# Kernel optimization log

Hardware: AMD Instinct MI355X
Metric: run time of the kernel (lower is better)

Reference implementation:

```python
import jax, jax.numpy as jnp
import numpy as np

EMBED = 1024
HEADS = 16
HEAD_DIM = EMBED // HEADS
HIDDEN = 4 * EMBED
EPS = 1e-6


def setup_inputs() -> dict:
    key = jax.random.key(0)
    ks = jax.random.split(key, 8)
    s = 0.02
    return {
        "x": jax.random.normal(ks[0], (2, 2048, EMBED), dtype=jnp.float32),
        "ln1_w": jnp.ones((EMBED,), jnp.float32),
        "ln1_b": jnp.zeros((EMBED,), jnp.float32),
        "qkv_w": jax.random.normal(ks[1], (3 * EMBED, EMBED), jnp.float32) * s,
        "qkv_b": jnp.zeros((3 * EMBED,), jnp.float32),
        "proj_w": jax.random.normal(ks[2], (EMBED, EMBED), jnp.float32) * s,
        "proj_b": jnp.zeros((EMBED,), jnp.float32),
        "ln2_w": jnp.ones((EMBED,), jnp.float32),
        "ln2_b": jnp.zeros((EMBED,), jnp.float32),
        "fc1_w": jax.random.normal(ks[3], (HIDDEN, EMBED), jnp.float32) * s,
        "fc1_b": jnp.zeros((HIDDEN,), jnp.float32),
        "fc2_w": jax.random.normal(ks[4], (EMBED, HIDDEN), jnp.float32) * s,
        "fc2_b": jnp.zeros((EMBED,), jnp.float32),
    }


def _layernorm(x, w, b):
    mu = jnp.mean(x, axis=-1, keepdims=True)
    var = jnp.mean(jnp.square(x - mu), axis=-1, keepdims=True)
    return (x - mu) * jax.lax.rsqrt(var + EPS) * w + b


def _attn(x, qkv_w, qkv_b, proj_w, proj_b):
    B, S, E = x.shape
    qkv = x @ qkv_w.T + qkv_b                      # [B,S,3E]
    qkv = qkv.reshape(B, S, 3, HEADS, HEAD_DIM)
    q, k, v = jnp.moveaxis(qkv, 2, 0)              # each [B,S,H,D]
    q = q.transpose(0, 2, 1, 3)                    # [B,H,S,D]
    k = k.transpose(0, 2, 1, 3)
    v = v.transpose(0, 2, 1, 3)
    scale = HEAD_DIM ** -0.5
    scores = jnp.einsum("bhqd,bhkd->bhqk", q, k) * scale
    mask = jnp.tril(jnp.ones((S, S), dtype=bool))
    scores = jnp.where(mask, scores, -jnp.inf)
    attn = jax.nn.softmax(scores, axis=-1)
    out = jnp.einsum("bhqk,bhkd->bhqd", attn, v)   # [B,H,S,D]
    out = out.transpose(0, 2, 1, 3).reshape(B, S, E)
    return out @ proj_w.T + proj_b


def reference(x, ln1_w, ln1_b, qkv_w, qkv_b, proj_w, proj_b,
              ln2_w, ln2_b, fc1_w, fc1_b, fc2_w, fc2_b):
    x = x + _attn(_layernorm(x, ln1_w, ln1_b), qkv_w, qkv_b, proj_w, proj_b)
    h = _layernorm(x, ln2_w, ln2_b)
    h = jax.nn.gelu(h @ fc1_w.T + fc1_b, approximate=False)
    x = x + (h @ fc2_w.T + fc2_b)
    return x
```

## Files before the change

kernel.cpp:

```cpp
#include <hip/hip_runtime.h>
#include <hip/hip_bf16.h>


#define E_    1024
#define TE_   3072
#define S_    2048
#define B_    2
#define H_    16
#define MROWS 4096

typedef __attribute__((ext_vector_type(8))) short bf16x8;
typedef __attribute__((ext_vector_type(4))) short short4v;
typedef __attribute__((ext_vector_type(4))) float f32x4;

__device__ __forceinline__ short f2bf(float f) {
  union { float f; unsigned u; } v; v.f = f;
  unsigned r = v.u + 0x7fffu + ((v.u >> 16) & 1u);
  return (short)(r >> 16);
}
__device__ __forceinline__ float bf2f(short s) {
  union { unsigned u; float f; } v; v.u = ((unsigned)(unsigned short)s) << 16;
  return v.f;
}
__device__ __forceinline__ void gload_lds16(const void* g, void* l) {
  __builtin_amdgcn_global_load_lds(
      (const __attribute__((address_space(1))) unsigned int*)g,
      (__attribute__((address_space(3))) unsigned int*)l, 16, 0, 0);
}
__device__ __forceinline__ float exp2_fast(float x) {
  float r; asm("v_exp_f32 %0, %1" : "=v"(r) : "v"(x)); return r;
}
__device__ __forceinline__ float gelu_f(float v) {
  return 0.5f * v * (1.0f + erff(v * 0.70710678118654752f));
}

__global__ __launch_bounds__(256) void k_cvt4(const float* __restrict__ i0, short* __restrict__ o0, int n0,
                                              const float* __restrict__ i1, short* __restrict__ o1, int n1,
                                              const float* __restrict__ i2, short* __restrict__ o2, int n2,
                                              const float* __restrict__ i3, short* __restrict__ o3, int n3) {
  const float* in; short* out; int n;
  switch (blockIdx.y) {
    case 0: in = i0; out = o0; n = n0; break;
    case 1: in = i1; out = o1; n = n1; break;
    case 2: in = i2; out = o2; n = n2; break;
    default: in = i3; out = o3; n = n3; break;
  }
  int i = blockIdx.x * 256 + threadIdx.x;
  if (i >= n) return;
  float4 v = ((const float4*)in)[i];
  short4v o = { f2bf(v.x), f2bf(v.y), f2bf(v.z), f2bf(v.w) };
  ((short4v*)out)[i] = o;
}

__global__ __launch_bounds__(256) void k_ln(const float* __restrict__ x,
                                            const float* __restrict__ w,
                                            const float* __restrict__ b,
                                            short* __restrict__ out) {
  int row = blockIdx.x;
  int tid = threadIdx.x;
  float4 v = ((const float4*)(x + (size_t)row * E_))[tid];
  float s  = v.x + v.y + v.z + v.w;
  float s2 = v.x*v.x + v.y*v.y + v.z*v.z + v.w*v.w;
  #pragma unroll
  for (int d = 1; d < 64; d <<= 1) { s += __shfl_xor(s, d); s2 += __shfl_xor(s2, d); }
  __shared__ float rs[4], rq[4];
  int wv = tid >> 6;
  if ((tid & 63) == 0) { rs[wv] = s; rq[wv] = s2; }
  __syncthreads();
  s  = rs[0] + rs[1] + rs[2] + rs[3];
  s2 = rq[0] + rq[1] + rq[2] + rq[3];
  float mu  = s * (1.0f / E_);
  float var = fmaxf(s2 * (1.0f / E_) - mu * mu, 0.0f);
  float inv = rsqrtf(var + 1e-6f);
  float4 wv4 = ((const float4*)w)[tid];
  float4 bv4 = ((const float4*)b)[tid];
  short4v o = { f2bf((v.x - mu) * inv * wv4.x + bv4.x),
                f2bf((v.y - mu) * inv * wv4.y + bv4.y),
                f2bf((v.z - mu) * inv * wv4.z + bv4.z),
                f2bf((v.w - mu) * inv * wv4.w + bv4.w) };
  ((short4v*)(out + (size_t)row * E_))[tid] = o;
}

template <int EPI>
__global__ __launch_bounds__(256, 3) void k_gemm(const short* __restrict__ A,
                                                 const short* __restrict__ W,
                                                 const float* __restrict__ bias,
                                                 const float* __restrict__ res,
                                                 void* __restrict__ outv,
                                                 int M, int N, int K) {
  __shared__ short As[2][128 * 32];
  __shared__ short Ws[2][128 * 32];
  int tid  = threadIdx.x;
  int lane = tid & 63, wave = tid >> 6;
  int wm = wave >> 1, wn = wave & 1;
  int m0 = blockIdx.y * 128, n0 = blockIdx.x * 128;
  int fr = lane & 15, fq = lane >> 4, fk = fq * 8;

  f32x4 acc[4][4];
  #pragma unroll
  for (int i = 0; i < 4; ++i)
    #pragma unroll
    for (int j = 0; j < 4; ++j) acc[i][j] = (f32x4){0.f, 0.f, 0.f, 0.f};

  int sr = tid >> 2;
  int sc = (tid & 3) * 8;
  const short* Arow  = A + (size_t)(m0 + sr) * K + sc;
  const short* Wrow  = W + (size_t)(n0 + sr) * K + sc;
  const short* Arow2 = A + (size_t)(m0 + 64 + sr) * K + sc;
  const short* Wrow2 = W + (size_t)(n0 + 64 + sr) * K + sc;

#define STAGE_(buf, k0)                                   \
  do {                                                    \
    gload_lds16(Arow  + (k0), &As[buf][tid * 8]);         \
    gload_lds16(Arow2 + (k0), &As[buf][2048 + tid * 8]);  \
    gload_lds16(Wrow  + (k0), &Ws[buf][tid * 8]);         \
    gload_lds16(Wrow2 + (k0), &Ws[buf][2048 + tid * 8]);  \
  } while (0)

#define COMPUTE_(buf)                                                         \
  do {                                                                        \
    bf16x8 af[4], bfr[4];                                                     \
    _Pragma("unroll")                                                         \
    for (int i = 0; i < 4; ++i) {                                             \
      af[i]  = *(const bf16x8*)(&As[buf][(wm * 64 + i * 16 + fr) * 32 + fk]); \
      bfr[i] = *(const bf16x8*)(&Ws[buf][(wn * 64 + i * 16 + fr) * 32 + fk]); \
    }                                                                         \
    _Pragma("unroll")                                                         \
    for (int mi = 0; mi < 4; ++mi)                                            \
      _Pragma("unroll")                                                       \
      for (int ni = 0; ni < 4; ++ni)                                          \
        acc[mi][ni] = __builtin_amdgcn_mfma_f32_16x16x32_bf16(                \
            af[mi], bfr[ni], acc[mi][ni], 0, 0, 0);                           \
  } while (0)

  int nt = K >> 5;
  STAGE_(0, 0);
  __syncthreads();
  int cur = 0;
  for (int t = 0; t < nt - 1; ++t) {
    STAGE_(cur ^ 1, (t + 1) * 32);
    COMPUTE_(cur);
    __syncthreads();
    cur ^= 1;
  }
  COMPUTE_(cur);

#undef STAGE_
#undef COMPUTE_

  #pragma unroll
  for (int mi = 0; mi < 4; ++mi) {
    #pragma unroll
    for (int ni = 0; ni < 4; ++ni) {
      int gm0 = m0 + wm * 64 + mi * 16 + fq * 4;
      int gn  = n0 + wn * 64 + ni * 16 + fr;
      float bv = bias[gn];
      #pragma unroll
      for (int j = 0; j < 4; ++j) {
        size_t idx = (size_t)(gm0 + j) * N + gn;
        float v = acc[mi][ni][j] + bv;
        if (EPI == 0)      ((short*)outv)[idx] = f2bf(v);
        else if (EPI == 1) ((float*)outv)[idx] = v + res[idx];
        else               ((short*)outv)[idx] = f2bf(gelu_f(v));
      }
    }
  }
}

__global__ __launch_bounds__(256, 3) void k_attn(const short* __restrict__ qkv,
                                                 short* __restrict__ out) {
  __shared__ short Kt[2][64 * 64];
  __shared__ short Vt[2][64 * 64];
  __shared__ short Pl[4][2048];
  int tid  = threadIdx.x;
  int lane = tid & 63, w = tid >> 6;
  int qb   = (int)gridDim.x - 1 - (int)blockIdx.x;
  int q0   = qb * 128;
  int bh   = blockIdx.y;
  int b    = bh >> 4, h = bh & 15;
  int fr   = lane & 15, fq = lane >> 4, fk = fq * 8;
  const float sc = 0.18033688011112042f;

  bf16x8 qa[2][2];
  #pragma unroll
  for (int g2 = 0; g2 < 2; ++g2) {
    const short* qp = qkv + (size_t)(b * S_ + q0 + w * 32 + g2 * 16 + fr) * TE_ + h * 64;
    qa[g2][0] = *(const bf16x8*)(qp + fk);
    qa[g2][1] = *(const bf16x8*)(qp + 32 + fk);
  }

  float m_r[2] = {-__builtin_inff(), -__builtin_inff()};
  float l_r[2] = {0.f, 0.f};
  f32x4 o[2][4];
  #pragma unroll
  for (int g2 = 0; g2 < 2; ++g2)
    #pragma unroll
    for (int c = 0; c < 4; ++c) o[g2][c] = (f32x4){0.f, 0.f, 0.f, 0.f};

  int srow = tid >> 3;
  int schunk = tid & 7;
  short* Pw = &Pl[w][0];
  bf16x8 vv[2];

#define V_LOAD_(kvv)                                                          \
  do {                                                                        \
    _Pragma("unroll")                                                         \
    for (int r = 0; r < 2; ++r) {                                             \
      size_t grow = (size_t)(b * S_ + (kvv) + srow + 32 * r) * TE_ + h * 64;  \
      vv[r] = *(const bf16x8*)(qkv + grow + 2 * E_ + (schunk << 3));          \
    }                                                                         \
  } while (0)

#define K_STAGE_(buf, kvv)                                                    \
  do {                                                                        \
    _Pragma("unroll")                                                         \
    for (int r = 0; r < 2; ++r) {                                             \
      size_t grow = (size_t)(b * S_ + (kvv) + srow + 32 * r) * TE_ + h * 64;  \
      gload_lds16(qkv + grow + E_ + ((schunk ^ (srow & 7)) << 3),             \
                  &Kt[buf][r * 2048 + tid * 8]);                              \
    }                                                                         \
  } while (0)

#define V_WRITE_(buf)                                                         \
  do {                                                                        \
    _Pragma("unroll")                                                         \
    for (int r = 0; r < 2; ++r) {                                             \
      int row = srow + 32 * r;                                                \
      int kc = row >> 3, kwi = row & 7;                                       \
      _Pragma("unroll")                                                       \
      for (int j = 0; j < 8; ++j) {                                           \
        int d = (schunk << 3) + j;                                            \
        int csw = kc ^ (d & 7) ^ ((d >> 3) & 7);                              \
        Vt[buf][d * 64 + csw * 8 + kwi] = vv[r][j];                           \
      }                                                                       \
    }                                                                         \
  } while (0)

  V_LOAD_(0);
  K_STAGE_(0, 0);
  V_WRITE_(0);
  __syncthreads();
  int cur = 0;
  int nt = 2 * qb + 2;

  for (int t = 0; t < nt; ++t) {
    int kv = t * 64;
    if (t + 1 < nt) {
      V_LOAD_((t + 1) * 64);
      K_STAGE_(cur ^ 1, (t + 1) * 64);
    }

    int sw = fr & 7;
    bf16x8 ka[4][2];
    #pragma unroll
    for (int g = 0; g < 4; ++g) {
      const short* kb = &Kt[cur][((g << 4) + fr) * 64];
      ka[g][0] = *(const bf16x8*)(kb + ((fq ^ sw) << 3));
      ka[g][1] = *(const bf16x8*)(kb + (((4 + fq) ^ sw) << 3));
    }
    f32x4 s[2][4];
    #pragma unroll
    for (int g2 = 0; g2 < 2; ++g2)
      #pragma unroll
      for (int g = 0; g < 4; ++g) {
        f32x4 t0 = (f32x4){0.f, 0.f, 0.f, 0.f};
        t0 = __builtin_amdgcn_mfma_f32_16x16x32_bf16(ka[g][0], qa[g2][0], t0, 0, 0, 0);
        t0 = __builtin_amdgcn_mfma_f32_16x16x32_bf16(ka[g][1], qa[g2][1], t0, 0, 0, 0);
        s[g2][g] = t0;
      }
    #pragma unroll
    for (int g2 = 0; g2 < 2; ++g2)
      #pragma unroll
      for (int g = 0; g < 4; ++g)
        #pragma unroll
        for (int jj = 0; jj < 4; ++jj) s[g2][g][jj] *= sc;

    if (kv + 64 > q0) {
      #pragma unroll
      for (int g2 = 0; g2 < 2; ++g2) {
        int qr = (q0 - kv) + 32 * w + 16 * g2 + fr;
        #pragma unroll
        for (int g = 0; g < 4; ++g)
          #pragma unroll
          for (int jj = 0; jj < 4; ++jj)
            if (16 * g + 4 * fq + jj > qr) s[g2][g][jj] = -__builtin_inff();
      }
    }

    #pragma unroll
    for (int g2 = 0; g2 < 2; ++g2) {
      float mg0 = fmaxf(fmaxf(s[g2][0][0], s[g2][0][1]), fmaxf(s[g2][0][2], s[g2][0][3]));
      float mg1 = fmaxf(fmaxf(s[g2][1][0], s[g2][1][1]), fmaxf(s[g2][1][2], s[g2][1][3]));
      float mg2 = fmaxf(fmaxf(s[g2][2][0], s[g2][2][1]), fmaxf(s[g2][2][2], s[g2][2][3]));
      float mg3 = fmaxf(fmaxf(s[g2][3][0], s[g2][3][1]), fmaxf(s[g2][3][2], s[g2][3][3]));
      float mt = fmaxf(fmaxf(mg0, mg1), fmaxf(mg2, mg3));
      mt = fmaxf(mt, __shfl_xor(mt, 16));
      mt = fmaxf(mt, __shfl_xor(mt, 32));
      float mn = fmaxf(m_r[g2], mt);
      float al = exp2_fast(m_r[g2] - mn);
      m_r[g2] = mn;
      #pragma unroll
      for (int g = 0; g < 4; ++g)
        #pragma unroll
        for (int jj = 0; jj < 4; ++jj) s[g2][g][jj] = exp2_fast(s[g2][g][jj] - mn);
      f32x4 s4 = s[g2][0] + s[g2][1] + s[g2][2] + s[g2][3];
      float ps = (s4[0] + s4[1]) + (s4[2] + s4[3]);
      ps += __shfl_xor(ps, 16);
      ps += __shfl_xor(ps, 32);
      l_r[g2] = l_r[g2] * al + ps;

      #pragma unroll
      for (int g = 0; g < 4; ++g) {
        short4v pk = { f2bf(s[g2][g][0]), f2bf(s[g2][g][1]),
                       f2bf(s[g2][g][2]), f2bf(s[g2][g][3]) };
        int pc = (2 * g + (fq >> 1)) ^ (fr & 7);
        *(short4v*)(Pw + g2 * 1024 + fr * 64 + pc * 8 + ((fq & 1) << 2)) = pk;
      }
      #pragma unroll
      for (int c = 0; c < 4; ++c)
        #pragma unroll
        for (int jj = 0; jj < 4; ++jj) o[g2][c][jj] *= al;
    }

    bf16x8 pb[2][2];
    #pragma unroll
    for (int g2 = 0; g2 < 2; ++g2) {
      pb[g2][0] = *(const bf16x8*)(Pw + g2 * 1024 + fr * 64 + ((fq ^ (fr & 7)) << 3));
      pb[g2][1] = *(const bf16x8*)(Pw + g2 * 1024 + fr * 64 + (((4 + fq) ^ (fr & 7)) << 3));
    }
    #pragma unroll
    for (int c = 0; c < 4; ++c) {
      int d = 16 * c + fr;
      int sbase = (d & 7) ^ ((d >> 3) & 7);
      const short* vb = &Vt[cur][d * 64];
      bf16x8 va0 = *(const bf16x8*)(vb + ((fq ^ sbase) << 3));
      bf16x8 va1 = *(const bf16x8*)(vb + (((4 + fq) ^ sbase) << 3));
      #pragma unroll
      for (int g2 = 0; g2 < 2; ++g2) {
        o[g2][c] = __builtin_amdgcn_mfma_f32_16x16x32_bf16(va0, pb[g2][0], o[g2][c], 0, 0, 0);
        o[g2][c] = __builtin_amdgcn_mfma_f32_16x16x32_bf16(va1, pb[g2][1], o[g2][c], 0, 0, 0);
      }
    }

    if (t + 1 < nt) V_WRITE_(cur ^ 1);
    __syncthreads();
    cur ^= 1;
  }

#undef V_LOAD_
#undef K_STAGE_
#undef V_WRITE_

  int ql = lane >> 2, dc = lane & 3;
  int swz = ql & 7;
  #pragma unroll
  for (int g2 = 0; g2 < 2; ++g2) {
    float inv_l = 1.0f / l_r[g2];
    #pragma unroll
    for (int c = 0; c < 4; ++c) {
      short4v okk = { f2bf(o[g2][c][0] * inv_l), f2bf(o[g2][c][1] * inv_l),
                      f2bf(o[g2][c][2] * inv_l), f2bf(o[g2][c][3] * inv_l) };
      int pc = (2 * c + (fq >> 1)) ^ (fr & 7);
      *(short4v*)(Pw + g2 * 1024 + fr * 64 + pc * 8 + ((fq & 1) << 2)) = okk;
    }
    const short* ob = Pw + g2 * 1024 + ql * 64;
    bf16x8 r0 = *(const bf16x8*)(ob + (((2 * dc) ^ swz) << 3));
    bf16x8 r1 = *(const bf16x8*)(ob + (((2 * dc + 1) ^ swz) << 3));
    short* op = out + (size_t)(b * S_ + q0 + 32 * w + 16 * g2 + ql) * E_ + h * 64 + dc * 16;
    *(bf16x8*)op = r0;
    *(bf16x8*)(op + 8) = r1;
  }
}

extern "C" void kernel_launch(void* const* d_in, const int* in_sizes, int n_in,
                              void* d_out, int out_size, void* d_ws, size_t ws_size,
                              hipStream_t stream) {
  const float* x      = (const float*)d_in[0];
  const float* ln1_w  = (const float*)d_in[1];
  const float* ln1_b  = (const float*)d_in[2];
  const float* qkv_w  = (const float*)d_in[3];
  const float* qkv_b  = (const float*)d_in[4];
  const float* proj_w = (const float*)d_in[5];
  const float* proj_b = (const float*)d_in[6];
  const float* ln2_w  = (const float*)d_in[7];
  const float* ln2_b  = (const float*)d_in[8];
  const float* fc1_w  = (const float*)d_in[9];
  const float* fc1_b  = (const float*)d_in[10];
  const float* fc2_w  = (const float*)d_in[11];
  const float* fc2_b  = (const float*)d_in[12];
  float* out = (float*)d_out;

  char* ws = (char*)d_ws;
  short* xn1    = (short*)(ws + 0);
  short* qkvb   = (short*)(ws + (8u  << 20));
  short* gelu_o = (short*)(ws + 0);
  short* attn_o = (short*)(ws + (32u << 20));
  short* h_ln2  = (short*)(ws + (32u << 20));
  float* x_res  = (float*)(ws + (40u << 20));
  short* w_qkv  = (short*)(ws + (56u << 20));
  short* w_proj = (short*)(ws + (62u << 20));
  short* w_fc1  = (short*)(ws + (64u << 20));
  short* w_fc2  = (short*)(ws + (72u << 20));

  k_cvt4<<<dim3(4096, 4), 256, 0, stream>>>(qkv_w, w_qkv, 786432,
                                            proj_w, w_proj, 262144,
                                            fc1_w, w_fc1, 1048576,
                                            fc2_w, w_fc2, 1048576);

  k_ln<<<MROWS, 256, 0, stream>>>(x, ln1_w, ln1_b, xn1);
  k_gemm<0><<<dim3(24, 32), 256, 0, stream>>>(xn1, w_qkv, qkv_b, nullptr, qkvb,
                                              MROWS, TE_, E_);
  k_attn<<<dim3(S_ / 128, B_ * H_), 256, 0, stream>>>(qkvb, attn_o);
  k_gemm<1><<<dim3(8, 32), 256, 0, stream>>>(attn_o, w_proj, proj_b, x, x_res,
                                             MROWS, E_, E_);
  k_ln<<<MROWS, 256, 0, stream>>>(x_res, ln2_w, ln2_b, h_ln2);
  k_gemm<2><<<dim3(32, 32), 256, 0, stream>>>(h_ln2, w_fc1, fc1_b, nullptr, gelu_o,
                                              MROWS, 4096, E_);
  k_gemm<1><<<dim3(8, 32), 256, 0, stream>>>(gelu_o, w_fc2, fc2_b, x_res, out,
                                             MROWS, E_, 4096);
}
```

Measured before the change: 396.4 us.

## Restructure GEMM: 512 threads, K=64 tiles, swizzled LDS, XCD-aware block remap

The GEMM kernel moves from 4 to 8 waves per block and doubles the K step to 64. It adds an XOR swizzle on LDS rows to avoid bank conflicts and remaps block IDs across the 8 XCDs for better L2 locality. It also replaces __syncthreads with explicit vmcnt/lgkmcnt waits and barriers so the next stage's loads overlap compute, and raises wave priority around the MFMA block. The intent is to cut LDS bank conflicts and global-load stalls, at the cost of more LDS per block (64KB) and fewer resident blocks.

```diff
diff --git a/kernel.cpp b/kernel.cpp
--- a/kernel.cpp
+++ b/kernel.cpp
@@ -82,67 +82,88 @@
 }
 
 template <int EPI>
-__global__ __launch_bounds__(256, 3) void k_gemm(const short* __restrict__ A,
+__global__ __launch_bounds__(512, 2) void k_gemm(const short* __restrict__ A,
                                                  const short* __restrict__ W,
                                                  const float* __restrict__ bias,
                                                  const float* __restrict__ res,
                                                  void* __restrict__ outv,
                                                  int M, int N, int K) {
-  __shared__ short As[2][128 * 32];
-  __shared__ short Ws[2][128 * 32];
+  __shared__ short As[2][8192];
+  __shared__ short Ws[2][8192];
   int tid  = threadIdx.x;
   int lane = tid & 63, wave = tid >> 6;
-  int wm = wave >> 1, wn = wave & 1;
-  int m0 = blockIdx.y * 128, n0 = blockIdx.x * 128;
-  int fr = lane & 15, fq = lane >> 4, fk = fq * 8;
-
-  f32x4 acc[4][4];
+  int wm = wave >> 2, wn = wave & 3;
+  int nwg = (int)(gridDim.x * gridDim.y);
+  int id  = (int)(blockIdx.y * gridDim.x + blockIdx.x);
+  int qc  = nwg >> 3;
+  int sid = (id & 7) * qc + (id >> 3);
+  int bx = sid % (int)gridDim.x, by = sid / (int)gridDim.x;
+  int m0 = by * 128, n0 = bx * 128;
+  int fr = lane & 15, fq = lane >> 4;
+  int fp = fr & 7;
+
+  f32x4 acc[4][2];
   #pragma unroll
   for (int i = 0; i < 4; ++i)
     #pragma unroll
-    for (int j = 0; j < 4; ++j) acc[i][j] = (f32x4){0.f, 0.f, 0.f, 0.f};
-
-  int sr = tid >> 2;
-  int sc = (tid & 3) * 8;
-  const short* Arow  = A + (size_t)(m0 + sr) * K + sc;
-  const short* Wrow  = W + (size_t)(n0 + sr) * K + sc;
-  const short* Arow2 = A + (size_t)(m0 + 64 + sr) * K + sc;
-  const short* Wrow2 = W + (size_t)(n0 + 64 + sr) * K + sc;
-
-#define STAGE_(buf, k0)                                   \
-  do {                                                    \
-    gload_lds16(Arow  + (k0), &As[buf][tid * 8]);         \
-    gload_lds16(Arow2 + (k0), &As[buf][2048 + tid * 8]);  \
-    gload_lds16(Wrow  + (k0), &Ws[buf][tid * 8]);         \
-    gload_lds16(Wrow2 + (k0), &Ws[buf][2048 + tid * 8]);  \
+    for (int j = 0; j < 2; ++j) acc[i][j] = (f32x4){0.f, 0.f, 0.f, 0.f};
+
+  int srow = tid >> 3;
+  int swz  = ((tid & 7) ^ (srow & 7)) << 3;
+  const short* Asrc = A + (size_t)(m0 + srow) * K + swz;
+  const short* Wsrc = W + (size_t)(n0 + srow) * K + swz;
+  size_t l64K = (size_t)64 * K;
+
+#define STAGE_(buf, k0)                                      \
+  do {                                                       \
+    gload_lds16(Asrc + (k0),        &As[buf][tid * 8]);      \
+    gload_lds16(Asrc + l64K + (k0), &As[buf][4096 + tid * 8]); \
+    gload_lds16(Wsrc + (k0),        &Ws[buf][tid * 8]);      \
+    gload_lds16(Wsrc + l64K + (k0), &Ws[buf][4096 + tid * 8]); \
   } while (0)
 
-#define COMPUTE_(buf)                                                         \
+#define COMPUTE_(bb)                                                          \
   do {                                                                        \
-    bf16x8 af[4], bfr[4];                                                     \
-    _Pragma("unroll")                                                         \
-    for (int i = 0; i < 4; ++i) {                                             \
-      af[i]  = *(const bf16x8*)(&As[buf][(wm * 64 + i * 16 + fr) * 32 + fk]); \
-      bfr[i] = *(const bf16x8*)(&Ws[buf][(wn * 64 + i * 16 + fr) * 32 + fk]); \
-    }                                                                         \
+    bf16x8 af[4][2], bfr[2][2];                                               \
     _Pragma("unroll")                                                         \
     for (int mi = 0; mi < 4; ++mi)                                            \
       _Pragma("unroll")                                                       \
-      for (int ni = 0; ni < 4; ++ni)                                          \
-        acc[mi][ni] = __builtin_amdgcn_mfma_f32_16x16x32_bf16(                \
-            af[mi], bfr[ni], acc[mi][ni], 0, 0, 0);                           \
+      for (int kk = 0; kk < 2; ++kk)                                          \
+        af[mi][kk] = *(const bf16x8*)(&As[bb][(wm * 64 + mi * 16 + fr) * 64 + \
+                                              (((kk << 2) + fq) ^ fp) * 8]);  \
+    _Pragma("unroll")                                                         \
+    for (int ni = 0; ni < 2; ++ni)                                            \
+      _Pragma("unroll")                                                       \
+      for (int kk = 0; kk < 2; ++kk)                                          \
+        bfr[ni][kk] = *(const bf16x8*)(&Ws[bb][(wn * 32 + ni * 16 + fr) * 64 + \
+                                               (((kk << 2) + fq) ^ fp) * 8]); \
+    __builtin_amdgcn_s_setprio(1);                                            \
+    _Pragma("unroll")                                                         \
+    for (int mi = 0; mi < 4; ++mi)                                            \
+      _Pragma("unroll")                                                       \
+      for (int ni = 0; ni < 2; ++ni)                                          \
+        _Pragma("unroll")                                                     \
+        for (int kk = 0; kk < 2; ++kk)                                        \
+          acc[mi][ni] = __builtin_amdgcn_mfma_f32_16x16x32_bf16(              \
+              af[mi][kk], bfr[ni][kk], acc[mi][ni], 0, 0, 0);                 \
+    __builtin_amdgcn_s_setprio(0);                                            \
   } while (0)
 
-  int nt = K >> 5;
+  int nt = K >> 6;
   STAGE_(0, 0);
-  __syncthreads();
+  STAGE_(1, 64);
   int cur = 0;
   for (int t = 0; t < nt - 1; ++t) {
-    STAGE_(cur ^ 1, (t + 1) * 32);
+    asm volatile("s_waitcnt vmcnt(4)" ::: "memory");
+    __builtin_amdgcn_s_barrier();
     COMPUTE_(cur);
-    __syncthreads();
+    asm volatile("s_waitcnt lgkmcnt(0)" ::: "memory");
+    __builtin_amdgcn_s_barrier();
+    if (t < nt - 2) STAGE_(cur, (size_t)(t + 2) * 64);
     cur ^= 1;
   }
+  asm volatile("s_waitcnt vmcnt(0)" ::: "memory");
+  __builtin_amdgcn_s_barrier();
   COMPUTE_(cur);
 
 #undef STAGE_
@@ -151,9 +172,9 @@
   #pragma unroll
   for (int mi = 0; mi < 4; ++mi) {
     #pragma unroll
-    for (int ni = 0; ni < 4; ++ni) {
+    for (int ni = 0; ni < 2; ++ni) {
       int gm0 = m0 + wm * 64 + mi * 16 + fq * 4;
-      int gn  = n0 + wn * 64 + ni * 16 + fr;
+      int gn  = n0 + wn * 32 + ni * 16 + fr;
       float bv = bias[gn];
       #pragma unroll
       for (int j = 0; j < 4; ++j) {
@@ -408,14 +429,14 @@
                                             fc2_w, w_fc2, 1048576);
 
   k_ln<<<MROWS, 256, 0, stream>>>(x, ln1_w, ln1_b, xn1);
-  k_gemm<0><<<dim3(24, 32), 256, 0, stream>>>(xn1, w_qkv, qkv_b, nullptr, qkvb,
+  k_gemm<0><<<dim3(24, 32), 512, 0, stream>>>(xn1, w_qkv, qkv_b, nullptr, qkvb,
                                               MROWS, TE_, E_);
   k_attn<<<dim3(S_ / 128, B_ * H_), 256, 0, stream>>>(qkvb, attn_o);
-  k_gemm<1><<<dim3(8, 32), 256, 0, stream>>>(attn_o, w_proj, proj_b, x, x_res,
+  k_gemm<1><<<dim3(8, 32), 512, 0, stream>>>(attn_o, w_proj, proj_b, x, x_res,
                                              MROWS, E_, E_);
   k_ln<<<MROWS, 256, 0, stream>>>(x_res, ln2_w, ln2_b, h_ln2);
-  k_gemm<2><<<dim3(32, 32), 256, 0, stream>>>(h_ln2, w_fc1, fc1_b, nullptr, gelu_o,
+  k_gemm<2><<<dim3(32, 32), 512, 0, stream>>>(h_ln2, w_fc1, fc1_b, nullptr, gelu_o,
                                               MROWS, 4096, E_);
-  k_gemm<1><<<dim3(8, 32), 256, 0, stream>>>(gelu_o, w_fc2, fc2_b, x_res, out,
+  k_gemm<1><<<dim3(8, 32), 512, 0, stream>>>(gelu_o, w_fc2, fc2_b, x_res, out,
                                              MROWS, E_, 4096);
 }
```

Result: faster. 373.7 us (-5.7%).
